# Kernel tuning notes

Hardware: AMD Instinct MI355X
Metric: run time of the kernel (lower is better)

The kernel has to match this reference:

```python
import jax, jax.numpy as jnp
import numpy as np

T, B, IN, H, L, A = 200, 16384, 2, 20, 2, 3  # seq, batch, input_dim, hidden, layers, actions


def setup_inputs() -> dict:
    key = jax.random.key(0)
    ks = jax.random.split(key, 12)
    s = 1.0 / np.sqrt(H)  # PyTorch LSTM init scale
    return {
        "x": jax.random.normal(ks[0], (T, B, IN), jnp.float32),
        "h0": jnp.zeros((L, B, H), jnp.float32),
        "c0": jnp.zeros((L, B, H), jnp.float32),
        "W_ih_0": jax.random.normal(ks[1], (4 * H, IN), jnp.float32) * s,
        "W_hh_0": jax.random.normal(ks[2], (4 * H, H), jnp.float32) * s,
        "b_ih_0": jax.random.normal(ks[3], (4 * H,), jnp.float32) * s,
        "b_hh_0": jax.random.normal(ks[4], (4 * H,), jnp.float32) * s,
        "W_ih_1": jax.random.normal(ks[5], (4 * H, H), jnp.float32) * s,
        "W_hh_1": jax.random.normal(ks[6], (4 * H, H), jnp.float32) * s,
        "b_ih_1": jax.random.normal(ks[7], (4 * H,), jnp.float32) * s,
        "b_hh_1": jax.random.normal(ks[8], (4 * H,), jnp.float32) * s,
        "W_dec": jax.random.normal(ks[9], (A, T * H), jnp.float32) * 0.02,
        "b_dec": jax.random.normal(ks[10], (A,), jnp.float32) * 0.02,
    }


def _lstm_layer(xs, h0, c0, W_ih, W_hh, b_ih, b_hh):
    # xs: [T, B, in]; precompute input projection for all steps at once.
    xw = jnp.einsum('tbi,gi->tbg', xs, W_ih) + b_ih  # [T, B, 4H]

    def step(carry, xw_t):
        h, c = carry
        gates = xw_t + h @ W_hh.T + b_hh  # [B, 4H]
        i, f, g, o = jnp.split(gates, 4, axis=-1)  # PyTorch gate order i,f,g,o
        c = jax.nn.sigmoid(f) * c + jax.nn.sigmoid(i) * jnp.tanh(g)
        h = jax.nn.sigmoid(o) * jnp.tanh(c)
        return (h, c), h

    (hT, cT), ys = jax.lax.scan(step, (h0, c0), xw)
    return ys, hT, cT  # ys: [T, B, H]


def reference(x, h0, c0, W_ih_0, W_hh_0, b_ih_0, b_hh_0,
              W_ih_1, W_hh_1, b_ih_1, b_hh_1, W_dec, b_dec):
    ys, h1, c1 = _lstm_layer(x, h0[0], c0[0], W_ih_0, W_hh_0, b_ih_0, b_hh_0)
    ys, h2, c2 = _lstm_layer(ys, h0[1], c0[1], W_ih_1, W_hh_1, b_ih_1, b_hh_1)
    # pad_packed_sequence(batch_first=True) -> [B, T, H], then flatten
    lstm_out = jnp.transpose(ys, (1, 0, 2)).reshape(ys.shape[1], -1)  # [B, T*H]
    logit = lstm_out @ W_dec.T + b_dec  # [B, A]
    log_prob = jax.nn.log_softmax(logit, axis=-1)
    # multinomial(1) from softmax(logit) == categorical sampling on logits
    action = jax.random.categorical(jax.random.key(42), logit, axis=-1)[:, None]  # [B,1] int
    selected_log_probs = jnp.take_along_axis(log_prob, action, axis=1)  # [B,1]
    h_n = jnp.stack([h1, h2])
    c_n = jnp.stack([c1, c2])
    return action, selected_log_probs, h_n, c_n
```

## Files before the change

kernel.cpp:

```cpp
#include <hip/hip_runtime.h>
#include <math.h>

#define TT 200
#define BB 16384
#define HH 20
#define EPB 64

#define OWI0P 0
#define OWH0P 160
#define OB0P  1760
#define OWI1P 1840
#define OWH1P 3440
#define OB1P  5040
#define SWN   5120

typedef float v2f __attribute__((ext_vector_type(2)));

__device__ double g_bd[3];

__device__ __forceinline__ void tf2x32(unsigned x0, unsigned x1,
                                       unsigned* o0, unsigned* o1) {
  const unsigned ks0 = 0u, ks1 = 42u;
  const unsigned ks2 = ks0 ^ ks1 ^ 0x1BD11BDAu;
  x0 += ks0; x1 += ks1;
#define ROTL_(v, d) (((v) << (d)) | ((v) >> (32 - (d))))
#define RND_(r) { x0 += x1; x1 = ROTL_(x1, r); x1 ^= x0; }
  RND_(13) RND_(15) RND_(26) RND_(6)
  x0 += ks1; x1 += ks2 + 1u;
  RND_(17) RND_(29) RND_(16) RND_(24)
  x0 += ks2; x1 += ks0 + 2u;
  RND_(13) RND_(15) RND_(26) RND_(6)
  x0 += ks0; x1 += ks1 + 3u;
  RND_(17) RND_(29) RND_(16) RND_(24)
  x0 += ks1; x1 += ks2 + 4u;
  RND_(13) RND_(15) RND_(26) RND_(6)
  x0 += ks2; x1 += ks0 + 5u;
  *o0 = x0; *o1 = x1;
#undef RND_
#undef ROTL_
}

__device__ __forceinline__ double bits2gumbel(unsigned bits) {
  float f = __uint_as_float((bits >> 9) | 0x3F800000u) - 1.0f;
  float uf = (f > 0.0f) ? f : 1.17549435e-38f;
  return -log(-log((double)uf));
}

__device__ __forceinline__ float sigm_f(float x) {
  float e = __expf(-x);
  return __builtin_amdgcn_rcpf(1.0f + e);
}
__device__ __forceinline__ float tanh_f(float x) {
  float e = __expf(2.0f * x);
  return 1.0f - 2.0f * __builtin_amdgcn_rcpf(1.0f + e);
}

__global__ void prep_kernel(const float* __restrict__ b_dec) {
  int i = threadIdx.x;
  if (i < 3) g_bd[i] = (double)g_bd[i] * 0.0 + (double)b_dec[i];
}

template <int NC>
__device__ __forceinline__ void l0_chunk(const float* __restrict__ sw, int u0,
                                         float x0a, float x1a,
                                         float x0b, float x1b,
                                         const float* hpA, const float* hpB,
                                         float* cA, float* cB,
                                         float* dstA, float* dstB) {
  v2f a01[NC], a23[NC], b01[NC], b23[NC];
#pragma unroll
  for (int u = 0; u < NC; ++u) {
    float4 b = *(const float4*)&sw[OB0P + (u0 + u) * 4];
    a01[u] = (v2f){b.x, b.y}; a23[u] = (v2f){b.z, b.w};
    b01[u] = (v2f){b.x, b.y}; b23[u] = (v2f){b.z, b.w};
  }
#pragma unroll
  for (int u = 0; u < NC; ++u) {
    float4 wa = *(const float4*)&sw[OWI0P + (u0 + u) * 8 + 0];
    float4 wb = *(const float4*)&sw[OWI0P + (u0 + u) * 8 + 4];
    a01[u] = __builtin_elementwise_fma((v2f){wa.x, wa.y}, (v2f){x0a, x0a}, a01[u]);
    a23[u] = __builtin_elementwise_fma((v2f){wa.z, wa.w}, (v2f){x0a, x0a}, a23[u]);
    b01[u] = __builtin_elementwise_fma((v2f){wa.x, wa.y}, (v2f){x0b, x0b}, b01[u]);
    b23[u] = __builtin_elementwise_fma((v2f){wa.z, wa.w}, (v2f){x0b, x0b}, b23[u]);
    a01[u] = __builtin_elementwise_fma((v2f){wb.x, wb.y}, (v2f){x1a, x1a}, a01[u]);
    a23[u] = __builtin_elementwise_fma((v2f){wb.z, wb.w}, (v2f){x1a, x1a}, a23[u]);
    b01[u] = __builtin_elementwise_fma((v2f){wb.x, wb.y}, (v2f){x1b, x1b}, b01[u]);
    b23[u] = __builtin_elementwise_fma((v2f){wb.z, wb.w}, (v2f){x1b, x1b}, b23[u]);
  }
#pragma unroll
  for (int j = 0; j < HH; ++j) {
    v2f ha = (v2f){hpA[j], hpA[j]};
    v2f hb = (v2f){hpB[j], hpB[j]};
#pragma unroll
    for (int u = 0; u < NC; ++u) {
      float4 w = *(const float4*)&sw[OWH0P + ((u0 + u) * HH + j) * 4];
      a01[u] = __builtin_elementwise_fma((v2f){w.x, w.y}, ha, a01[u]);
      a23[u] = __builtin_elementwise_fma((v2f){w.z, w.w}, ha, a23[u]);
      b01[u] = __builtin_elementwise_fma((v2f){w.x, w.y}, hb, b01[u]);
      b23[u] = __builtin_elementwise_fma((v2f){w.z, w.w}, hb, b23[u]);
    }
  }
#pragma unroll
  for (int u = 0; u < NC; ++u) {
    { float si = sigm_f(a01[u].x), sf = sigm_f(a01[u].y);
      float tg = tanh_f(a23[u].x), so = sigm_f(a23[u].y);
      float c = fmaf(sf, cA[u], si * tg);
      cA[u] = c; dstA[u] = so * tanh_f(c); }
    { float si = sigm_f(b01[u].x), sf = sigm_f(b01[u].y);
      float tg = tanh_f(b23[u].x), so = sigm_f(b23[u].y);
      float c = fmaf(sf, cB[u], si * tg);
      cB[u] = c; dstB[u] = so * tanh_f(c); }
  }
}

__device__ __forceinline__ void l1_chunk2(const float* __restrict__ sw, int u0,
                                          const float* hpA, const float* hpB,
                                          const float* h1A, const float* h1B,
                                          float* cA, float* cB,
                                          float* dstA, float* dstB,
                                          double wd00, double wd01,
                                          double wd10, double wd11,
                                          double wd20, double wd21,
                                          double* lgA, double* lgB) {
  v2f a01[2], a23[2], b01[2], b23[2];
#pragma unroll
  for (int u = 0; u < 2; ++u) {
    float4 b = *(const float4*)&sw[OB1P + (u0 + u) * 4];
    a01[u] = (v2f){b.x, b.y}; a23[u] = (v2f){b.z, b.w};
    b01[u] = (v2f){b.x, b.y}; b23[u] = (v2f){b.z, b.w};
  }
#pragma unroll
  for (int j = 0; j < HH; ++j) {
    v2f ha = (v2f){hpA[j], hpA[j]};
    v2f hb = (v2f){hpB[j], hpB[j]};
#pragma unroll
    for (int u = 0; u < 2; ++u) {
      float4 w = *(const float4*)&sw[OWI1P + ((u0 + u) * HH + j) * 4];
      a01[u] = __builtin_elementwise_fma((v2f){w.x, w.y}, ha, a01[u]);
      a23[u] = __builtin_elementwise_fma((v2f){w.z, w.w}, ha, a23[u]);
      b01[u] = __builtin_elementwise_fma((v2f){w.x, w.y}, hb, b01[u]);
      b23[u] = __builtin_elementwise_fma((v2f){w.z, w.w}, hb, b23[u]);
    }
  }
#pragma unroll
  for (int j = 0; j < HH; ++j) {
    v2f ha = (v2f){h1A[j], h1A[j]};
    v2f hb = (v2f){h1B[j], h1B[j]};
#pragma unroll
    for (int u = 0; u < 2; ++u) {
      float4 w = *(const float4*)&sw[OWH1P + ((u0 + u) * HH + j) * 4];
      a01[u] = __builtin_elementwise_fma((v2f){w.x, w.y}, ha, a01[u]);
      a23[u] = __builtin_elementwise_fma((v2f){w.z, w.w}, ha, a23[u]);
      b01[u] = __builtin_elementwise_fma((v2f){w.x, w.y}, hb, b01[u]);
      b23[u] = __builtin_elementwise_fma((v2f){w.z, w.w}, hb, b23[u]);
    }
  }
#pragma unroll
  for (int u = 0; u < 2; ++u) {
    { float si = sigm_f(a01[u].x), sf = sigm_f(a01[u].y);
      float tg = tanh_f(a23[u].x), so = sigm_f(a23[u].y);
      float c = fmaf(sf, cA[u], si * tg);
      cA[u] = c;
      float h = so * tanh_f(c);
      dstA[u] = h;
      double hd = (double)h;
      if (u == 0) { lgA[0] = fma(wd00, hd, lgA[0]); lgA[1] = fma(wd10, hd, lgA[1]); lgA[2] = fma(wd20, hd, lgA[2]); }
      else        { lgA[0] = fma(wd01, hd, lgA[0]); lgA[1] = fma(wd11, hd, lgA[1]); lgA[2] = fma(wd21, hd, lgA[2]); } }
    { float si = sigm_f(b01[u].x), sf = sigm_f(b01[u].y);
      float tg = tanh_f(b23[u].x), so = sigm_f(b23[u].y);
      float c = fmaf(sf, cB[u], si * tg);
      cB[u] = c;
      float h = so * tanh_f(c);
      dstB[u] = h;
      double hd = (double)h;
      if (u == 0) { lgB[0] = fma(wd00, hd, lgB[0]); lgB[1] = fma(wd10, hd, lgB[1]); lgB[2] = fma(wd20, hd, lgB[2]); }
      else        { lgB[0] = fma(wd01, hd, lgB[0]); lgB[1] = fma(wd11, hd, lgB[1]); lgB[2] = fma(wd21, hd, lgB[2]); } }
  }
}

__global__ __launch_bounds__(512, 2) void lstm_wave_kernel(
    const float* __restrict__ x,
    const float* __restrict__ h0_in,
    const float* __restrict__ c0_in,
    const float* __restrict__ Wih0,
    const float* __restrict__ Whh0,
    const float* __restrict__ bih0,
    const float* __restrict__ bhh0,
    const float* __restrict__ Wih1,
    const float* __restrict__ Whh1,
    const float* __restrict__ bih1,
    const float* __restrict__ bhh1,
    const float* __restrict__ Wdec_f,
    float* __restrict__ out) {
  __shared__ float s_h0[2][EPB][22];
  __shared__ float s_h1[2][EPB][22];
  __shared__ double s_logit[10][EPB][3];
  __shared__ __align__(16) float s_w[SWN];

  const int tid = threadIdx.x;
  const int lane = tid & 63;
  const int wv = __builtin_amdgcn_readfirstlane((int)(tid >> 6));
  const int e = lane & 31;
  const int hf = lane >> 5;
  const int eg0 = blockIdx.x * EPB + e;
  const int eg1 = eg0 + 32;

  for (int i = tid; i < SWN; i += 512) {
    float v;
    if (i < OWH0P) {
      int g = i & 3, t = i >> 2, j = t & 1, u = t >> 1;
      v = Wih0[(g * 20 + u) * 2 + j];
    } else if (i < OB0P) {
      int k = i - OWH0P, g = k & 3, t = k >> 2, j = t % 20, u = t / 20;
      v = Whh0[(g * 20 + u) * 20 + j];
    } else if (i < OWI1P) {
      int k = i - OB0P, g = k & 3, u = k >> 2;
      v = bih0[g * 20 + u] + bhh0[g * 20 + u];
    } else if (i < OWH1P) {
      int k = i - OWI1P, g = k & 3, t = k >> 2, j = t % 20, u = t / 20;
      v = Wih1[(g * 20 + u) * 20 + j];
    } else if (i < OB1P) {
      int k = i - OWH1P, g = k & 3, t = k >> 2, j = t % 20, u = t / 20;
      v = Whh1[(g * 20 + u) * 20 + j];
    } else {
      int k = i - OB1P, g = k & 3, u = k >> 2;
      v = bih1[g * 20 + u] + bhh1[g * 20 + u];
    }
    s_w[i] = v;
  }

  const bool isL0 = (wv < 3);
  int u0, nu;
  if (isL0) {
    if (wv == 0) { u0 = hf * 4;               nu = 4; }
    else         { u0 = 8 + (wv - 1) * 6 + hf * 3; nu = 3; }
  } else {
    u0 = (wv - 3) * 4 + hf * 2; nu = 2;
  }

  float cA[4], cB[4];
  double lgA[3] = {0.0, 0.0, 0.0};
  double lgB[3] = {0.0, 0.0, 0.0};

  {
    const int l = isL0 ? 0 : 1;
#pragma unroll
    for (int u = 0; u < 4; ++u) {
      if (u < nu) {
        cA[u] = c0_in[l * BB * HH + eg0 * HH + u0 + u];
        cB[u] = c0_in[l * BB * HH + eg1 * HH + u0 + u];
        float hA = h0_in[l * BB * HH + eg0 * HH + u0 + u];
        float hB = h0_in[l * BB * HH + eg1 * HH + u0 + u];
        if (isL0) { s_h0[1][e][u0 + u] = hA; s_h0[1][e + 32][u0 + u] = hB; }
        else      { s_h1[1][e][u0 + u] = hA; s_h1[1][e + 32][u0 + u] = hB; }
      }
    }
  }
  __syncthreads();

  const float2* x2 = (const float2*)x;
  const float2* wd2 = (const float2*)Wdec_f;

  float2 xvA_cur, xvB_cur;
  if (isL0) { xvA_cur = x2[0 * BB + eg0]; xvB_cur = x2[0 * BB + eg1]; }

  for (int s = 0; s <= TT; ++s) {
    if (isL0) {
      if (s < TT) {
        const int rb = (s + 1) & 1;
        const int wb = s & 1;
        float2 xvA = xvA_cur, xvB = xvB_cur;
        if (s + 1 < TT) {
          xvA_cur = x2[(s + 1) * BB + eg0];
          xvB_cur = x2[(s + 1) * BB + eg1];
        }
        float hpA[HH], hpB[HH];
#pragma unroll
        for (int j2 = 0; j2 < 10; ++j2) {
          float2 vA = *(const float2*)&s_h0[rb][e][2 * j2];
          float2 vB = *(const float2*)&s_h0[rb][e + 32][2 * j2];
          hpA[2 * j2] = vA.x; hpA[2 * j2 + 1] = vA.y;
          hpB[2 * j2] = vB.x; hpB[2 * j2 + 1] = vB.y;
        }
        float* dstA = &s_h0[wb][e][u0];
        float* dstB = &s_h0[wb][e + 32][u0];
        if (wv == 0) l0_chunk<4>(s_w, u0, xvA.x, xvA.y, xvB.x, xvB.y, hpA, hpB, cA, cB, dstA, dstB);
        else         l0_chunk<3>(s_w, u0, xvA.x, xvA.y, xvB.x, xvB.y, hpA, hpB, cA, cB, dstA, dstB);
      }
    } else {
      if (s >= 1) {
        const int t1 = s - 1;
        const int h0b = t1 & 1;
        const int h1rb = (t1 + 1) & 1;
        const int col = t1 * HH + u0;
        float2 w0 = wd2[(0    + col) >> 1];
        float2 w1 = wd2[(4000 + col) >> 1];
        float2 w2 = wd2[(8000 + col) >> 1];
        float hpA[HH], hpB[HH], h1A[HH], h1B[HH];
#pragma unroll
        for (int j2 = 0; j2 < 10; ++j2) {
          float2 vA = *(const float2*)&s_h0[h0b][e][2 * j2];
          float2 vB = *(const float2*)&s_h0[h0b][e + 32][2 * j2];
          hpA[2 * j2] = vA.x; hpA[2 * j2 + 1] = vA.y;
          hpB[2 * j2] = vB.x; hpB[2 * j2 + 1] = vB.y;
          float2 uA = *(const float2*)&s_h1[h1rb][e][2 * j2];
          float2 uB = *(const float2*)&s_h1[h1rb][e + 32][2 * j2];
          h1A[2 * j2] = uA.x; h1A[2 * j2 + 1] = uA.y;
          h1B[2 * j2] = uB.x; h1B[2 * j2 + 1] = uB.y;
        }
        float* dstA = &s_h1[h0b][e][u0];
        float* dstB = &s_h1[h0b][e + 32][u0];
        l1_chunk2(s_w, u0, hpA, hpB, h1A, h1B, cA, cB, dstA, dstB,
                  (double)w0.x, (double)w0.y,
                  (double)w1.x, (double)w1.y,
                  (double)w2.x, (double)w2.y, lgA, lgB);
      }
    }
    __syncthreads();
  }

  {
    const int l = isL0 ? 0 : 1;
#pragma unroll
    for (int u = 0; u < 4; ++u) {
      if (u < nu) {
        float hA = isL0 ? s_h0[1][e][u0 + u] : s_h1[1][e][u0 + u];
        float hB = isL0 ? s_h0[1][e + 32][u0 + u] : s_h1[1][e + 32][u0 + u];
        out[2 * BB + l * BB * HH + eg0 * HH + u0 + u] = hA;
        out[2 * BB + l * BB * HH + eg1 * HH + u0 + u] = hB;
        out[2 * BB + 2 * BB * HH + l * BB * HH + eg0 * HH + u0 + u] = cA[u];
        out[2 * BB + 2 * BB * HH + l * BB * HH + eg1 * HH + u0 + u] = cB[u];
      }
    }
  }

  if (!isL0) {
    const int k = (wv - 3) * 2 + hf;
    s_logit[k][e][0] = lgA[0];
    s_logit[k][e][1] = lgA[1];
    s_logit[k][e][2] = lgA[2];
    s_logit[k][e + 32][0] = lgB[0];
    s_logit[k][e + 32][1] = lgB[1];
    s_logit[k][e + 32][2] = lgB[2];
  }
  __syncthreads();

  if (wv == 0) {
    const int ed = lane;
    const int egd = blockIdx.x * EPB + ed;
    double l[3];
#pragma unroll
    for (int a = 0; a < 3; ++a) {
      double v = g_bd[a];
#pragma unroll
      for (int k = 0; k < 10; ++k) v += s_logit[k][ed][a];
      l[a] = v;
    }

    int act = 0;
    double vbest = -1.0e300;
#pragma unroll
    for (int a = 0; a < 3; ++a) {
      unsigned idx = 3u * (unsigned)egd + (unsigned)a;
      unsigned p0, p1;
      tf2x32(0u, idx, &p0, &p1);
      double g = bits2gumbel(p0 ^ p1);
      double v = l[a] + g;
      if (v > vbest) { vbest = v; act = a; }
    }
    double m = fmax(l[0], fmax(l[1], l[2]));
    double se = exp(l[0] - m) + exp(l[1] - m) + exp(l[2] - m);
    double lp = (l[act] - m) - log(se);
    out[egd] = (float)act;
    out[BB + egd] = (float)lp;
  }
}

extern "C" void kernel_launch(void* const* d_in, const int* in_sizes, int n_in,
                              void* d_out, int out_size, void* d_ws, size_t ws_size,
                              hipStream_t stream) {
  prep_kernel<<<dim3(1), dim3(64), 0, stream>>>((const float*)d_in[12]);
  lstm_wave_kernel<<<dim3(BB / EPB), dim3(512), 0, stream>>>(
      (const float*)d_in[0], (const float*)d_in[1], (const float*)d_in[2],
      (const float*)d_in[3], (const float*)d_in[4],
      (const float*)d_in[5], (const float*)d_in[6],
      (const float*)d_in[7], (const float*)d_in[8],
      (const float*)d_in[9], (const float*)d_in[10],
      (const float*)d_in[11], (float*)d_out);
}
```

Baseline: 719.1 us.

## Move layer-1 weights to global scalar memory and remap layer-1 lanes per element

```diff
diff --git a/kernel.cpp b/kernel.cpp
--- a/kernel.cpp
+++ b/kernel.cpp
@@ -9,13 +9,16 @@
 #define OWI0P 0
 #define OWH0P 160
 #define OB0P  1760
-#define OWI1P 1840
-#define OWH1P 3440
-#define OB1P  5040
-#define SWN   5120
+#define SWN0  1840
+
+#define GWI1 0
+#define GWH1 1600
+#define GB1  3200
+#define GWN  3280
 
 typedef float v2f __attribute__((ext_vector_type(2)));
 
+__device__ float g_wpk[GWN];
 __device__ double g_bd[3];
 
 __device__ __forceinline__ void tf2x32(unsigned x0, unsigned x1,
@@ -55,9 +58,23 @@
   return 1.0f - 2.0f * __builtin_amdgcn_rcpf(1.0f + e);
 }
 
-__global__ void prep_kernel(const float* __restrict__ b_dec) {
-  int i = threadIdx.x;
-  if (i < 3) g_bd[i] = (double)g_bd[i] * 0.0 + (double)b_dec[i];
+__global__ void prep_kernel(const float* __restrict__ Wih1,
+                            const float* __restrict__ Whh1,
+                            const float* __restrict__ bih1,
+                            const float* __restrict__ bhh1,
+                            const float* __restrict__ b_dec) {
+  int i = blockIdx.x * 256 + threadIdx.x;
+  if (i < 3) g_bd[i] = (double)b_dec[i];
+  if (i < GWH1) {
+    int g = i & 3, t = i >> 2, j = t % 20, u = t / 20;
+    g_wpk[i] = Wih1[(g * 20 + u) * 20 + j];
+  } else if (i < GB1) {
+    int k = i - GWH1, g = k & 3, t = k >> 2, j = t % 20, u = t / 20;
+    g_wpk[i] = Whh1[(g * 20 + u) * 20 + j];
+  } else if (i < GWN) {
+    int k = i - GB1, g = k & 3, u = k >> 2;
+    g_wpk[i] = bih1[g * 20 + u] + bhh1[g * 20 + u];
+  }
 }
 
 template <int NC>
@@ -113,68 +130,53 @@
   }
 }
 
-__device__ __forceinline__ void l1_chunk2(const float* __restrict__ sw, int u0,
-                                          const float* hpA, const float* hpB,
-                                          const float* h1A, const float* h1B,
-                                          float* cA, float* cB,
-                                          float* dstA, float* dstB,
-                                          double wd00, double wd01,
-                                          double wd10, double wd11,
-                                          double wd20, double wd21,
-                                          double* lgA, double* lgB) {
-  v2f a01[2], a23[2], b01[2], b23[2];
-#pragma unroll
-  for (int u = 0; u < 2; ++u) {
-    float4 b = *(const float4*)&sw[OB1P + (u0 + u) * 4];
+__device__ __forceinline__ void l1_quad(const float* __restrict__ gw, int u0,
+                                        const float* hp0, const float* h1r,
+                                        float* c_st, float* dst,
+                                        float4 w0, float4 w1, float4 w2,
+                                        double* lgA, double* lgB) {
+  v2f a01[4], a23[4];
+#pragma unroll
+  for (int u = 0; u < 4; ++u) {
+    float4 b = *(const float4*)&gw[GB1 + (u0 + u) * 4];
     a01[u] = (v2f){b.x, b.y}; a23[u] = (v2f){b.z, b.w};
-    b01[u] = (v2f){b.x, b.y}; b23[u] = (v2f){b.z, b.w};
   }
 #pragma unroll
   for (int j = 0; j < HH; ++j) {
-    v2f ha = (v2f){hpA[j], hpA[j]};
-    v2f hb = (v2f){hpB[j], hpB[j]};
-#pragma unroll
-    for (int u = 0; u < 2; ++u) {
-      float4 w = *(const float4*)&sw[OWI1P + ((u0 + u) * HH + j) * 4];
-      a01[u] = __builtin_elementwise_fma((v2f){w.x, w.y}, ha, a01[u]);
-      a23[u] = __builtin_elementwise_fma((v2f){w.z, w.w}, ha, a23[u]);
-      b01[u] = __builtin_elementwise_fma((v2f){w.x, w.y}, hb, b01[u]);
-      b23[u] = __builtin_elementwise_fma((v2f){w.z, w.w}, hb, b23[u]);
+    v2f hb = (v2f){hp0[j], hp0[j]};
+#pragma unroll
+    for (int u = 0; u < 4; ++u) {
+      float4 w = *(const float4*)&gw[GWI1 + ((u0 + u) * HH + j) * 4];
+      a01[u] = __builtin_elementwise_fma((v2f){w.x, w.y}, hb, a01[u]);
+      a23[u] = __builtin_elementwise_fma((v2f){w.z, w.w}, hb, a23[u]);
     }
   }
 #pragma unroll
   for (int j = 0; j < HH; ++j) {
-    v2f ha = (v2f){h1A[j], h1A[j]};
-    v2f hb = (v2f){h1B[j], h1B[j]};
-#pragma unroll
-    for (int u = 0; u < 2; ++u) {
-      float4 w = *(const float4*)&sw[OWH1P + ((u0 + u) * HH + j) * 4];
-      a01[u] = __builtin_elementwise_fma((v2f){w.x, w.y}, ha, a01[u]);
-      a23[u] = __builtin_elementwise_fma((v2f){w.z, w.w}, ha, a23[u]);
-      b01[u] = __builtin_elementwise_fma((v2f){w.x, w.y}, hb, b01[u]);
-      b23[u] = __builtin_elementwise_fma((v2f){w.z, w.w}, hb, b23[u]);
-    }
-  }
-#pragma unroll
-  for (int u = 0; u < 2; ++u) {
-    { float si = sigm_f(a01[u].x), sf = sigm_f(a01[u].y);
-      float tg = tanh_f(a23[u].x), so = sigm_f(a23[u].y);
-      float c = fmaf(sf, cA[u], si * tg);
-      cA[u] = c;
-      float h = so * tanh_f(c);
-      dstA[u] = h;
-      double hd = (double)h;
-      if (u == 0) { lgA[0] = fma(wd00, hd, lgA[0]); lgA[1] = fma(wd10, hd, lgA[1]); lgA[2] = fma(wd20, hd, lgA[2]); }
-      else        { lgA[0] = fma(wd01, hd, lgA[0]); lgA[1] = fma(wd11, hd, lgA[1]); lgA[2] = fma(wd21, hd, lgA[2]); } }
-    { float si = sigm_f(b01[u].x), sf = sigm_f(b01[u].y);
-      float tg = tanh_f(b23[u].x), so = sigm_f(b23[u].y);
-      float c = fmaf(sf, cB[u], si * tg);
-      cB[u] = c;
-      float h = so * tanh_f(c);
-      dstB[u] = h;
-      double hd = (double)h;
-      if (u == 0) { lgB[0] = fma(wd00, hd, lgB[0]); lgB[1] = fma(wd10, hd, lgB[1]); lgB[2] = fma(wd20, hd, lgB[2]); }
-      else        { lgB[0] = fma(wd01, hd, lgB[0]); lgB[1] = fma(wd11, hd, lgB[1]); lgB[2] = fma(wd21, hd, lgB[2]); } }
+    v2f hb = (v2f){h1r[j], h1r[j]};
+#pragma unroll
+    for (int u = 0; u < 4; ++u) {
+      float4 w = *(const float4*)&gw[GWH1 + ((u0 + u) * HH + j) * 4];
+      a01[u] = __builtin_elementwise_fma((v2f){w.x, w.y}, hb, a01[u]);
+      a23[u] = __builtin_elementwise_fma((v2f){w.z, w.w}, hb, a23[u]);
+    }
+  }
+#pragma unroll
+  for (int u = 0; u < 4; ++u) {
+    float si = sigm_f(a01[u].x), sf = sigm_f(a01[u].y);
+    float tg = tanh_f(a23[u].x), so = sigm_f(a23[u].y);
+    float c = fmaf(sf, c_st[u], si * tg);
+    c_st[u] = c;
+    float h = so * tanh_f(c);
+    dst[u] = h;
+    double hd = (double)h;
+    double* lg = (u < 2) ? lgA : lgB;
+    float f0 = (u == 0) ? w0.x : (u == 1) ? w0.y : (u == 2) ? w0.z : w0.w;
+    float f1 = (u == 0) ? w1.x : (u == 1) ? w1.y : (u == 2) ? w1.z : w1.w;
+    float f2 = (u == 0) ? w2.x : (u == 1) ? w2.y : (u == 2) ? w2.z : w2.w;
+    lg[0] = fma((double)f0, hd, lg[0]);
+    lg[1] = fma((double)f1, hd, lg[1]);
+    lg[2] = fma((double)f2, hd, lg[2]);
   }
 }
 
@@ -186,16 +188,12 @@
     const float* __restrict__ Whh0,
     const float* __restrict__ bih0,
     const float* __restrict__ bhh0,
-    const float* __restrict__ Wih1,
-    const float* __restrict__ Whh1,
-    const float* __restrict__ bih1,
-    const float* __restrict__ bhh1,
     const float* __restrict__ Wdec_f,
     float* __restrict__ out) {
   __shared__ float s_h0[2][EPB][22];
   __shared__ float s_h1[2][EPB][22];
   __shared__ double s_logit[10][EPB][3];
-  __shared__ __align__(16) float s_w[SWN];
+  __shared__ __align__(16) float s_w[SWN0];
 
   const int tid = threadIdx.x;
   const int lane = tid & 63;
@@ -204,8 +202,10 @@
   const int hf = lane >> 5;
   const int eg0 = blockIdx.x * EPB + e;
   const int eg1 = eg0 + 32;
-
-  for (int i = tid; i < SWN; i += 512) {
+  const int el = lane;
+  const int egl = blockIdx.x * EPB + el;
+
+  for (int i = tid; i < SWN0; i += 512) {
     float v;
     if (i < OWH0P) {
       int g = i & 3, t = i >> 2, j = t & 1, u = t >> 1;
@@ -213,18 +213,9 @@
     } else if (i < OB0P) {
       int k = i - OWH0P, g = k & 3, t = k >> 2, j = t % 20, u = t / 20;
       v = Whh0[(g * 20 + u) * 20 + j];
-    } else if (i < OWI1P) {
+    } else {
       int k = i - OB0P, g = k & 3, u = k >> 2;
       v = bih0[g * 20 + u] + bhh0[g * 20 + u];
-    } else if (i < OWH1P) {
-      int k = i - OWI1P, g = k & 3, t = k >> 2, j = t % 20, u = t / 20;
-      v = Wih1[(g * 20 + u) * 20 + j];
-    } else if (i < OB1P) {
-      int k = i - OWH1P, g = k & 3, t = k >> 2, j = t % 20, u = t / 20;
-      v = Whh1[(g * 20 + u) * 20 + j];
-    } else {
-      int k = i - OB1P, g = k & 3, u = k >> 2;
-      v = bih1[g * 20 + u] + bhh1[g * 20 + u];
     }
     s_w[i] = v;
   }
@@ -232,34 +223,37 @@
   const bool isL0 = (wv < 3);
   int u0, nu;
   if (isL0) {
-    if (wv == 0) { u0 = hf * 4;               nu = 4; }
-    else         { u0 = 8 + (wv - 1) * 6 + hf * 3; nu = 3; }
+    if (wv == 0) { u0 = hf * 4;                     nu = 4; }
+    else         { u0 = 8 + (wv - 1) * 6 + hf * 3;  nu = 3; }
   } else {
-    u0 = (wv - 3) * 4 + hf * 2; nu = 2;
+    u0 = __builtin_amdgcn_readfirstlane((wv - 3) * 4); nu = 4;
   }
 
   float cA[4], cB[4];
   double lgA[3] = {0.0, 0.0, 0.0};
   double lgB[3] = {0.0, 0.0, 0.0};
 
-  {
-    const int l = isL0 ? 0 : 1;
+  if (isL0) {
 #pragma unroll
     for (int u = 0; u < 4; ++u) {
       if (u < nu) {
-        cA[u] = c0_in[l * BB * HH + eg0 * HH + u0 + u];
-        cB[u] = c0_in[l * BB * HH + eg1 * HH + u0 + u];
-        float hA = h0_in[l * BB * HH + eg0 * HH + u0 + u];
-        float hB = h0_in[l * BB * HH + eg1 * HH + u0 + u];
-        if (isL0) { s_h0[1][e][u0 + u] = hA; s_h0[1][e + 32][u0 + u] = hB; }
-        else      { s_h1[1][e][u0 + u] = hA; s_h1[1][e + 32][u0 + u] = hB; }
+        cA[u] = c0_in[eg0 * HH + u0 + u];
+        cB[u] = c0_in[eg1 * HH + u0 + u];
+        s_h0[1][e][u0 + u] = h0_in[eg0 * HH + u0 + u];
+        s_h0[1][e + 32][u0 + u] = h0_in[eg1 * HH + u0 + u];
       }
     }
+  } else {
+#pragma unroll
+    for (int u = 0; u < 4; ++u) {
+      cA[u] = c0_in[BB * HH + egl * HH + u0 + u];
+      s_h1[1][el][u0 + u] = h0_in[BB * HH + egl * HH + u0 + u];
+    }
   }
   __syncthreads();
 
   const float2* x2 = (const float2*)x;
-  const float2* wd2 = (const float2*)Wdec_f;
+  const float4* wdq = (const float4*)Wdec_f;
 
   float2 xvA_cur, xvB_cur;
   if (isL0) { xvA_cur = x2[0 * BB + eg0]; xvB_cur = x2[0 * BB + eg1]; }
@@ -293,55 +287,47 @@
         const int h0b = t1 & 1;
         const int h1rb = (t1 + 1) & 1;
         const int col = t1 * HH + u0;
-        float2 w0 = wd2[(0    + col) >> 1];
-        float2 w1 = wd2[(4000 + col) >> 1];
-        float2 w2 = wd2[(8000 + col) >> 1];
-        float hpA[HH], hpB[HH], h1A[HH], h1B[HH];
+        float4 w0 = wdq[(0    + col) >> 2];
+        float4 w1 = wdq[(4000 + col) >> 2];
+        float4 w2 = wdq[(8000 + col) >> 2];
+        float hp0[HH], h1r[HH];
 #pragma unroll
         for (int j2 = 0; j2 < 10; ++j2) {
-          float2 vA = *(const float2*)&s_h0[h0b][e][2 * j2];
-          float2 vB = *(const float2*)&s_h0[h0b][e + 32][2 * j2];
-          hpA[2 * j2] = vA.x; hpA[2 * j2 + 1] = vA.y;
-          hpB[2 * j2] = vB.x; hpB[2 * j2 + 1] = vB.y;
-          float2 uA = *(const float2*)&s_h1[h1rb][e][2 * j2];
-          float2 uB = *(const float2*)&s_h1[h1rb][e + 32][2 * j2];
-          h1A[2 * j2] = uA.x; h1A[2 * j2 + 1] = uA.y;
-          h1B[2 * j2] = uB.x; h1B[2 * j2 + 1] = uB.y;
+          float2 vA = *(const float2*)&s_h0[h0b][el][2 * j2];
+          float2 uA = *(const float2*)&s_h1[h1rb][el][2 * j2];
+          hp0[2 * j2] = vA.x; hp0[2 * j2 + 1] = vA.y;
+          h1r[2 * j2] = uA.x; h1r[2 * j2 + 1] = uA.y;
         }
-        float* dstA = &s_h1[h0b][e][u0];
-        float* dstB = &s_h1[h0b][e + 32][u0];
-        l1_chunk2(s_w, u0, hpA, hpB, h1A, h1B, cA, cB, dstA, dstB,
-                  (double)w0.x, (double)w0.y,
-                  (double)w1.x, (double)w1.y,
-                  (double)w2.x, (double)w2.y, lgA, lgB);
+        float* dst = &s_h1[h0b][el][u0];
+        l1_quad(g_wpk, u0, hp0, h1r, cA, dst, w0, w1, w2, lgA, lgB);
       }
     }
     __syncthreads();
   }
 
-  {
-    const int l = isL0 ? 0 : 1;
+  if (isL0) {
 #pragma unroll
     for (int u = 0; u < 4; ++u) {
       if (u < nu) {
-        float hA = isL0 ? s_h0[1][e][u0 + u] : s_h1[1][e][u0 + u];
-        float hB = isL0 ? s_h0[1][e + 32][u0 + u] : s_h1[1][e + 32][u0 + u];
-        out[2 * BB + l * BB * HH + eg0 * HH + u0 + u] = hA;
-        out[2 * BB + l * BB * HH + eg1 * HH + u0 + u] = hB;
-        out[2 * BB + 2 * BB * HH + l * BB * HH + eg0 * HH + u0 + u] = cA[u];
-        out[2 * BB + 2 * BB * HH + l * BB * HH + eg1 * HH + u0 + u] = cB[u];
+        out[2 * BB + eg0 * HH + u0 + u] = s_h0[1][e][u0 + u];
+        out[2 * BB + eg1 * HH + u0 + u] = s_h0[1][e + 32][u0 + u];
+        out[2 * BB + 2 * BB * HH + eg0 * HH + u0 + u] = cA[u];
+        out[2 * BB + 2 * BB * HH + eg1 * HH + u0 + u] = cB[u];
       }
     }
-  }
-
-  if (!isL0) {
-    const int k = (wv - 3) * 2 + hf;
-    s_logit[k][e][0] = lgA[0];
-    s_logit[k][e][1] = lgA[1];
-    s_logit[k][e][2] = lgA[2];
-    s_logit[k][e + 32][0] = lgB[0];
-    s_logit[k][e + 32][1] = lgB[1];
-    s_logit[k][e + 32][2] = lgB[2];
+  } else {
+#pragma unroll
+    for (int u = 0; u < 4; ++u) {
+      out[2 * BB + BB * HH + egl * HH + u0 + u] = s_h1[1][el][u0 + u];
+      out[2 * BB + 2 * BB * HH + BB * HH + egl * HH + u0 + u] = cA[u];
+    }
+    const int k0 = (wv - 3) * 2;
+    s_logit[k0][el][0] = lgA[0];
+    s_logit[k0][el][1] = lgA[1];
+    s_logit[k0][el][2] = lgA[2];
+    s_logit[k0 + 1][el][0] = lgB[0];
+    s_logit[k0 + 1][el][1] = lgB[1];
+    s_logit[k0 + 1][el][2] = lgB[2];
   }
   __syncthreads();
 
@@ -379,12 +365,13 @@
 extern "C" void kernel_launch(void* const* d_in, const int* in_sizes, int n_in,
                               void* d_out, int out_size, void* d_ws, size_t ws_size,
                               hipStream_t stream) {
-  prep_kernel<<<dim3(1), dim3(64), 0, stream>>>((const float*)d_in[12]);
+  prep_kernel<<<dim3((GWN + 255) / 256), dim3(256), 0, stream>>>(
+      (const float*)d_in[7], (const float*)d_in[8],
+      (const float*)d_in[9], (const float*)d_in[10],
+      (const float*)d_in[12]);
   lstm_wave_kernel<<<dim3(BB / EPB), dim3(512), 0, stream>>>(
       (const float*)d_in[0], (const float*)d_in[1], (const float*)d_in[2],
       (const float*)d_in[3], (const float*)d_in[4],
       (const float*)d_in[5], (const float*)d_in[6],
-      (const float*)d_in[7], (const float*)d_in[8],
-      (const float*)d_in[9], (const float*)d_in[10],
       (const float*)d_in[11], (float*)d_out);
 }
```

Measured after the change: 1.429 ms. 98.8% more time.

## Give layer-1 waves 6-7 four units per element with wave-uniform weights

Applied to the files above, without the earlier changes.

```diff
diff --git a/kernel.cpp b/kernel.cpp
--- a/kernel.cpp
+++ b/kernel.cpp
@@ -57,7 +57,7 @@
 
 __global__ void prep_kernel(const float* __restrict__ b_dec) {
   int i = threadIdx.x;
-  if (i < 3) g_bd[i] = (double)g_bd[i] * 0.0 + (double)b_dec[i];
+  if (i < 3) g_bd[i] = (double)b_dec[i];
 }
 
 template <int NC>
@@ -178,6 +178,56 @@
   }
 }
 
+__device__ __forceinline__ void l1_quad_smem(
+    const float* __restrict__ Wih1, const float* __restrict__ Whh1,
+    const float* __restrict__ bih1, const float* __restrict__ bhh1,
+    int u0, const float* hp0, const float* h1r, float* c_st, float* dst,
+    float4 w0, float4 w1, float4 w2, double* lgA, double* lgB) {
+  float acc[4][4];
+#pragma unroll
+  for (int u = 0; u < 4; ++u)
+#pragma unroll
+    for (int g = 0; g < 4; ++g) {
+      int row = g * 20 + u0 + u;
+      acc[u][g] = bih1[row] + bhh1[row];
+    }
+#pragma unroll
+  for (int j = 0; j < HH; ++j) {
+    float hj = hp0[j];
+#pragma unroll
+    for (int u = 0; u < 4; ++u)
+#pragma unroll
+      for (int g = 0; g < 4; ++g)
+        acc[u][g] = fmaf(Wih1[(g * 20 + u0 + u) * HH + j], hj, acc[u][g]);
+  }
+#pragma unroll
+  for (int j = 0; j < HH; ++j) {
+    float hj = h1r[j];
+#pragma unroll
+    for (int u = 0; u < 4; ++u)
+#pragma unroll
+      for (int g = 0; g < 4; ++g)
+        acc[u][g] = fmaf(Whh1[(g * 20 + u0 + u) * HH + j], hj, acc[u][g]);
+  }
+#pragma unroll
+  for (int u = 0; u < 4; ++u) {
+    float si = sigm_f(acc[u][0]), sf = sigm_f(acc[u][1]);
+    float tg = tanh_f(acc[u][2]), so = sigm_f(acc[u][3]);
+    float c = fmaf(sf, c_st[u], si * tg);
+    c_st[u] = c;
+    float h = so * tanh_f(c);
+    dst[u] = h;
+    double hd = (double)h;
+    double* lg = (u < 2) ? lgA : lgB;
+    float f0 = (u == 0) ? w0.x : (u == 1) ? w0.y : (u == 2) ? w0.z : w0.w;
+    float f1 = (u == 0) ? w1.x : (u == 1) ? w1.y : (u == 2) ? w1.z : w1.w;
+    float f2 = (u == 0) ? w2.x : (u == 1) ? w2.y : (u == 2) ? w2.z : w2.w;
+    lg[0] = fma((double)f0, hd, lg[0]);
+    lg[1] = fma((double)f1, hd, lg[1]);
+    lg[2] = fma((double)f2, hd, lg[2]);
+  }
+}
+
 __global__ __launch_bounds__(512, 2) void lstm_wave_kernel(
     const float* __restrict__ x,
     const float* __restrict__ h0_in,
@@ -204,6 +254,8 @@
   const int hf = lane >> 5;
   const int eg0 = blockIdx.x * EPB + e;
   const int eg1 = eg0 + 32;
+  const int el = lane;
+  const int egl = blockIdx.x * EPB + el;
 
   for (int i = tid; i < SWN; i += 512) {
     float v;
@@ -230,36 +282,51 @@
   }
 
   const bool isL0 = (wv < 3);
+  const bool isSm = (wv >= 6);
   int u0, nu;
   if (isL0) {
-    if (wv == 0) { u0 = hf * 4;               nu = 4; }
+    if (wv == 0) { u0 = hf * 4;                    nu = 4; }
     else         { u0 = 8 + (wv - 1) * 6 + hf * 3; nu = 3; }
+  } else if (!isSm) {
+    u0 = (wv - 3) * 4 + hf * 2; nu = 2;
   } else {
-    u0 = (wv - 3) * 4 + hf * 2; nu = 2;
+    u0 = __builtin_amdgcn_readfirstlane(12 + (wv - 6) * 4); nu = 4;
   }
 
   float cA[4], cB[4];
   double lgA[3] = {0.0, 0.0, 0.0};
   double lgB[3] = {0.0, 0.0, 0.0};
 
-  {
-    const int l = isL0 ? 0 : 1;
+  if (isL0) {
 #pragma unroll
     for (int u = 0; u < 4; ++u) {
       if (u < nu) {
-        cA[u] = c0_in[l * BB * HH + eg0 * HH + u0 + u];
-        cB[u] = c0_in[l * BB * HH + eg1 * HH + u0 + u];
-        float hA = h0_in[l * BB * HH + eg0 * HH + u0 + u];
-        float hB = h0_in[l * BB * HH + eg1 * HH + u0 + u];
-        if (isL0) { s_h0[1][e][u0 + u] = hA; s_h0[1][e + 32][u0 + u] = hB; }
-        else      { s_h1[1][e][u0 + u] = hA; s_h1[1][e + 32][u0 + u] = hB; }
+        cA[u] = c0_in[eg0 * HH + u0 + u];
+        cB[u] = c0_in[eg1 * HH + u0 + u];
+        s_h0[1][e][u0 + u] = h0_in[eg0 * HH + u0 + u];
+        s_h0[1][e + 32][u0 + u] = h0_in[eg1 * HH + u0 + u];
       }
+    }
+  } else if (!isSm) {
+#pragma unroll
+    for (int u = 0; u < 2; ++u) {
+      cA[u] = c0_in[BB * HH + eg0 * HH + u0 + u];
+      cB[u] = c0_in[BB * HH + eg1 * HH + u0 + u];
+      s_h1[1][e][u0 + u] = h0_in[BB * HH + eg0 * HH + u0 + u];
+      s_h1[1][e + 32][u0 + u] = h0_in[BB * HH + eg1 * HH + u0 + u];
+    }
+  } else {
+#pragma unroll
+    for (int u = 0; u < 4; ++u) {
+      cA[u] = c0_in[BB * HH + egl * HH + u0 + u];
+      s_h1[1][el][u0 + u] = h0_in[BB * HH + egl * HH + u0 + u];
     }
   }
   __syncthreads();
 
   const float2* x2 = (const float2*)x;
   const float2* wd2 = (const float2*)Wdec_f;
+  const float4* wdq = (const float4*)Wdec_f;
 
   float2 xvA_cur, xvB_cur;
   if (isL0) { xvA_cur = x2[0 * BB + eg0]; xvB_cur = x2[0 * BB + eg1]; }
@@ -287,7 +354,7 @@
         if (wv == 0) l0_chunk<4>(s_w, u0, xvA.x, xvA.y, xvB.x, xvB.y, hpA, hpB, cA, cB, dstA, dstB);
         else         l0_chunk<3>(s_w, u0, xvA.x, xvA.y, xvB.x, xvB.y, hpA, hpB, cA, cB, dstA, dstB);
       }
-    } else {
+    } else if (!isSm) {
       if (s >= 1) {
         const int t1 = s - 1;
         const int h0b = t1 & 1;
@@ -315,26 +382,49 @@
                   (double)w1.x, (double)w1.y,
                   (double)w2.x, (double)w2.y, lgA, lgB);
       }
+    } else {
+      if (s >= 1) {
+        const int t1 = s - 1;
+        const int h0b = t1 & 1;
+        const int h1rb = (t1 + 1) & 1;
+        const int col = t1 * HH + u0;
+        float4 w0 = wdq[(0    + col) >> 2];
+        float4 w1 = wdq[(4000 + col) >> 2];
+        float4 w2 = wdq[(8000 + col) >> 2];
+        float hp0[HH], h1r[HH];
+#pragma unroll
+        for (int j2 = 0; j2 < 10; ++j2) {
+          float2 vA = *(const float2*)&s_h0[h0b][el][2 * j2];
+          float2 uA = *(const float2*)&s_h1[h1rb][el][2 * j2];
+          hp0[2 * j2] = vA.x; hp0[2 * j2 + 1] = vA.y;
+          h1r[2 * j2] = uA.x; h1r[2 * j2 + 1] = uA.y;
+        }
+        float* dst = &s_h1[h0b][el][u0];
+        l1_quad_smem(Wih1, Whh1, bih1, bhh1, u0, hp0, h1r, cA, dst,
+                     w0, w1, w2, lgA, lgB);
+      }
     }
     __syncthreads();
   }
 
-  {
-    const int l = isL0 ? 0 : 1;
+  if (isL0) {
 #pragma unroll
     for (int u = 0; u < 4; ++u) {
       if (u < nu) {
-        float hA = isL0 ? s_h0[1][e][u0 + u] : s_h1[1][e][u0 + u];
-        float hB = isL0 ? s_h0[1][e + 32][u0 + u] : s_h1[1][e + 32][u0 + u];
-        out[2 * BB + l * BB * HH + eg0 * HH + u0 + u] = hA;
-        out[2 * BB + l * BB * HH + eg1 * HH + u0 + u] = hB;
-        out[2 * BB + 2 * BB * HH + l * BB * HH + eg0 * HH + u0 + u] = cA[u];
-        out[2 * BB + 2 * BB * HH + l * BB * HH + eg1 * HH + u0 + u] = cB[u];
+        out[2 * BB + eg0 * HH + u0 + u] = s_h0[1][e][u0 + u];
+        out[2 * BB + eg1 * HH + u0 + u] = s_h0[1][e + 32][u0 + u];
+        out[2 * BB + 2 * BB * HH + eg0 * HH + u0 + u] = cA[u];
+        out[2 * BB + 2 * BB * HH + eg1 * HH + u0 + u] = cB[u];
       }
     }
-  }
-
-  if (!isL0) {
+  } else if (!isSm) {
+#pragma unroll
+    for (int u = 0; u < 2; ++u) {
+      out[2 * BB + BB * HH + eg0 * HH + u0 + u] = s_h1[1][e][u0 + u];
+      out[2 * BB + BB * HH + eg1 * HH + u0 + u] = s_h1[1][e + 32][u0 + u];
+      out[2 * BB + 2 * BB * HH + BB * HH + eg0 * HH + u0 + u] = cA[u];
+      out[2 * BB + 2 * BB * HH + BB * HH + eg1 * HH + u0 + u] = cB[u];
+    }
     const int k = (wv - 3) * 2 + hf;
     s_logit[k][e][0] = lgA[0];
     s_logit[k][e][1] = lgA[1];
@@ -342,6 +432,19 @@
     s_logit[k][e + 32][0] = lgB[0];
     s_logit[k][e + 32][1] = lgB[1];
     s_logit[k][e + 32][2] = lgB[2];
+  } else {
+#pragma unroll
+    for (int u = 0; u < 4; ++u) {
+      out[2 * BB + BB * HH + egl * HH + u0 + u] = s_h1[1][el][u0 + u];
+      out[2 * BB + 2 * BB * HH + BB * HH + egl * HH + u0 + u] = cA[u];
+    }
+    const int k0 = 6 + (wv - 6) * 2;
+    s_logit[k0][el][0] = lgA[0];
+    s_logit[k0][el][1] = lgA[1];
+    s_logit[k0][el][2] = lgA[2];
+    s_logit[k0 + 1][el][0] = lgB[0];
+    s_logit[k0 + 1][el][1] = lgB[1];
+    s_logit[k0 + 1][el][2] = lgB[2];
   }
   __syncthreads();
 
```

New measurement: 1.182 ms. 64.3% more time.
